# Kernel tuning notes

Measured on AMD Instinct MI355X. Metric: run time of the kernel, lower is better.

## Reference

```python
import jax, jax.numpy as jnp
import numpy as np

N, E, F_IN, F_E, H, T = 100000, 1600000, 128, 16, 64, 32
NEG_SLOPE = 0.2


def setup_inputs() -> dict:
    key = jax.random.key(0)
    ks = jax.random.split(key, 24)
    s = 0.1
    inp = {
        'x': jax.random.normal(ks[0], (N, F_IN), jnp.float32),
        'edge_index': jax.random.randint(ks[1], (2, E), 0, N, dtype=jnp.int32),
        'edge_attr': jax.random.normal(ks[2], (E, F_E), jnp.float32),
        # GATConv layer 1 (heads=1)
        'W1': jax.random.normal(ks[3], (F_IN, H), jnp.float32) * s,
        'as1': jax.random.normal(ks[4], (H,), jnp.float32) * s,
        'ad1': jax.random.normal(ks[5], (H,), jnp.float32) * s,
        'We1': jax.random.normal(ks[6], (F_E, H), jnp.float32) * s,
        'ae1': jax.random.normal(ks[7], (H,), jnp.float32) * s,
        'b1': jnp.zeros((H,), jnp.float32),
        # GATConv layer 2
        'W2': jax.random.normal(ks[8], (H, H), jnp.float32) * s,
        'as2': jax.random.normal(ks[9], (H,), jnp.float32) * s,
        'ad2': jax.random.normal(ks[10], (H,), jnp.float32) * s,
        'We2': jax.random.normal(ks[11], (F_E, H), jnp.float32) * s,
        'ae2': jax.random.normal(ks[12], (H,), jnp.float32) * s,
        'b2': jnp.zeros((H,), jnp.float32),
        # classifier MLP (dropout in eval mode -> identity)
        'Wc1': jax.random.normal(ks[13], (H, H // 2), jnp.float32) * s,
        'bc1': jnp.zeros((H // 2,), jnp.float32),
        'Wc2': jax.random.normal(ks[14], (H // 2, T), jnp.float32) * s,
        'bc2': jnp.zeros((T,), jnp.float32),
    }
    return inp


def gat_conv(x, src, dst, edge_attr, W, a_s, a_d, We, a_e, b):
    """Single-head PyG-style GATConv with edge features and self-loops
    (self-loop edge_attr = mean of incoming edge_attr, fill_value='mean')."""
    n = x.shape[0]
    # self loops with mean incoming edge features
    deg = jax.ops.segment_sum(jnp.ones_like(dst, jnp.float32), dst, n)
    loop_attr = jax.ops.segment_sum(edge_attr, dst, n) / jnp.maximum(deg, 1.0)[:, None]
    loops = jnp.arange(n, dtype=src.dtype)
    src_f = jnp.concatenate([src, loops])
    dst_f = jnp.concatenate([dst, loops])
    ea = jnp.concatenate([edge_attr, loop_attr], axis=0)  # [E+N, F_E]
    h = x @ W                                             # [N, H]
    # attention logits per edge: alpha_src[j] + alpha_dst[i] + alpha_edge
    alpha = (h @ a_s)[src_f] + (h @ a_d)[dst_f] + (ea @ We) @ a_e
    alpha = jax.nn.leaky_relu(alpha, NEG_SLOPE)
    # segment softmax over incoming edges per destination node
    m = jax.ops.segment_max(alpha, dst_f, n)
    p = jnp.exp(alpha - m[dst_f])
    z = jax.ops.segment_sum(p, dst_f, n)
    w = p / z[dst_f]                                      # [E+N]
    out = jax.ops.segment_sum(w[:, None] * h[src_f], dst_f, n)
    return out + b


def reference(x, edge_index, edge_attr, W1, as1, ad1, We1, ae1, b1,
              W2, as2, ad2, We2, ae2, b2, Wc1, bc1, Wc2, bc2):
    src, dst = edge_index[0], edge_index[1]
    h = jax.nn.relu(gat_conv(x, src, dst, edge_attr, W1, as1, ad1, We1, ae1, b1))
    h = jax.nn.relu(gat_conv(h, src, dst, edge_attr, W2, as2, ad2, We2, ae2, b2))
    h = jax.nn.relu(h @ Wc1 + bc1)
    logits = h @ Wc2 + bc2
    return logits
```

## Files before the change

### kernel.cpp

```cpp
#include <hip/hip_runtime.h>
#include <hip/hip_bf16.h>
#include <hip/hip_fp16.h>

#define NEG_SLOPE 0.2f
#define EPB 2048
#define NBUK 512

__device__ __forceinline__ float leaky(float a) { return a > 0.f ? a : NEG_SLOPE * a; }

__global__ __launch_bounds__(256) void count_pack(
    const int* __restrict__ dst, const float* __restrict__ eattr,
    const float* __restrict__ We1, const float* __restrict__ ae1,
    const float* __restrict__ We2, const float* __restrict__ ae2,
    unsigned int* __restrict__ meta_pay, int* __restrict__ counts, int E) {
    __shared__ float wvs[32];
    __shared__ int hist[NBUK];
    int tid = threadIdx.x, i = blockIdx.x;
    if (tid < 32) {
        const float* Wp = (tid < 16) ? We1 : We2;
        const float* ap = (tid < 16) ? ae1 : ae2;
        int f = tid & 15;
        float s = 0.f;
        for (int k = 0; k < 64; ++k) s += Wp[f * 64 + k] * ap[k];
        wvs[tid] = s;
    }
    for (int t = tid; t < NBUK; t += 256) hist[t] = 0;
    __syncthreads();
    int e0 = i * EPB, e1 = min(E, e0 + EPB);
    for (int e = e0 + tid; e < e1; e += 256) {
        int d = dst[e];
        atomicAdd(&hist[d >> 8], 1);
        const float4* ep = (const float4*)(eattr + (size_t)e * 16);
        float4 q0 = ep[0], q1 = ep[1], q2 = ep[2], q3 = ep[3];
        float a[16] = {q0.x, q0.y, q0.z, q0.w, q1.x, q1.y, q1.z, q1.w,
                       q2.x, q2.y, q2.z, q2.w, q3.x, q3.y, q3.z, q3.w};
        float s1 = 0.f, s2 = 0.f;
#pragma unroll
        for (int f = 0; f < 16; ++f) { s1 += a[f] * wvs[f]; s2 += a[f] * wvs[16 + f]; }
        unsigned int p1 = (unsigned int)__half_as_ushort(__float2half_rn(s1));
        unsigned int p2 = (unsigned int)__half_as_ushort(__float2half_rn(s2));
        meta_pay[e] = p1 | (p2 << 16);
    }
    __syncthreads();
    for (int t = tid; t < NBUK; t += 256) counts[(size_t)i * NBUK + t] = hist[t];
}

__global__ __launch_bounds__(1024) void scan_cols(const int* __restrict__ counts,
                                                  int* __restrict__ offsets,
                                                  int* __restrict__ btot, int nblk) {
    __shared__ int sh[1024];
    int b = blockIdx.x, t = threadIdx.x;
    int v = (t < nblk) ? counts[(size_t)t * NBUK + b] : 0;
    sh[t] = v;
    __syncthreads();
    for (int off = 1; off < 1024; off <<= 1) {
        int u = (t >= off) ? sh[t - off] : 0;
        __syncthreads();
        sh[t] += u;
        __syncthreads();
    }
    if (t < nblk) offsets[(size_t)t * NBUK + b] = sh[t] - v;
    if (t == 1023) btot[b] = sh[1023];
}

__global__ void scan_buckets(const int* __restrict__ btot, int* __restrict__ bbase,
                             int* __restrict__ rowptr, int E, int n) {
    __shared__ int sh[NBUK];
    int t = threadIdx.x;
    int v = btot[t];
    sh[t] = v;
    __syncthreads();
    for (int off = 1; off < NBUK; off <<= 1) {
        int u = (t >= off) ? sh[t - off] : 0;
        __syncthreads();
        sh[t] += u;
        __syncthreads();
    }
    bbase[t] = sh[t] - v;
    if (t == 0) rowptr[n] = E;
}

__global__ __launch_bounds__(256) void scatter_buckets(
    const int* __restrict__ dst, const int* __restrict__ src,
    const unsigned int* __restrict__ meta_pay, const int* __restrict__ offsets,
    const int* __restrict__ bbase, uint2* __restrict__ bucketed, int E) {
    __shared__ int cur[NBUK];
    int i = blockIdx.x, tid = threadIdx.x;
    for (int t = tid; t < NBUK; t += 256) cur[t] = bbase[t] + offsets[(size_t)i * NBUK + t];
    __syncthreads();
    int e0 = i * EPB, e1 = min(E, e0 + EPB);
    for (int e = e0 + tid; e < e1; e += 256) {
        int d = dst[e];
        int slot = atomicAdd(&cur[d >> 8], 1);
        bucketed[slot] = make_uint2((unsigned int)src[e] | ((unsigned int)(d & 255) << 24),
                                    meta_pay[e]);
    }
}

__global__ __launch_bounds__(256) void csr_build(const uint2* __restrict__ bucketed,
                                                 const int* __restrict__ bbase,
                                                 const int* __restrict__ btot,
                                                 int* __restrict__ rowptr,
                                                 uint2* __restrict__ recs, int n) {
    __shared__ int deg[256], sc[256], cur[256];
    int b = blockIdx.x, tid = threadIdx.x;
    int base = bbase[b], cnt = btot[b];
    deg[tid] = 0;
    __syncthreads();
    for (int k = tid; k < cnt; k += 256) {
        uint2 r = bucketed[base + k];
        atomicAdd(&deg[r.x >> 24], 1);
    }
    __syncthreads();
    int dv = deg[tid];
    sc[tid] = dv;
    __syncthreads();
    for (int off = 1; off < 256; off <<= 1) {
        int u = (tid >= off) ? sc[tid - off] : 0;
        __syncthreads();
        sc[tid] += u;
        __syncthreads();
    }
    int excl = sc[tid] - dv;
    int d = b * 256 + tid;
    if (d < n) rowptr[d] = base + excl;
    cur[tid] = base + excl;
    __syncthreads();
    for (int k = tid; k < cnt; k += 256) {
        uint2 r = bucketed[base + k];
        int dl = (int)(r.x >> 24);
        int pos = atomicAdd(&cur[dl], 1);
        recs[pos] = make_uint2(r.x & 0x00FFFFFFu, r.y);
    }
}

template <int K>
__global__ __launch_bounds__(256) void gemm_node(const float* __restrict__ X,
                                                 const float* __restrict__ W,
                                                 const float* __restrict__ a_s,
                                                 const float* __restrict__ a_d,
                                                 __half* __restrict__ Hout16,
                                                 float* __restrict__ ash,
                                                 float* __restrict__ adh, int n) {
    constexpr int KC = 64;
    __shared__ float xs[128 * 65];
    __shared__ float ws[KC * 64];
    int tid = threadIdx.x;
    int base = blockIdx.x * 128;
    int ct = tid & 7;
    int rt = tid >> 3;

    float acc[4][8];
#pragma unroll
    for (int i = 0; i < 4; ++i)
#pragma unroll
        for (int j = 0; j < 8; ++j) acc[i][j] = 0.f;

    for (int kc = 0; kc < K; kc += KC) {
#pragma unroll
        for (int p = 0; p < 8; ++p) {
            int idx = p * 256 + tid;
            int row = idx >> 4;
            int f4 = idx & 15;
            float4 q = make_float4(0.f, 0.f, 0.f, 0.f);
            if (base + row < n) q = *(const float4*)(X + (size_t)(base + row) * K + kc + f4 * 4);
            float* dp = xs + row * 65 + f4 * 4;
            dp[0] = q.x; dp[1] = q.y; dp[2] = q.z; dp[3] = q.w;
        }
#pragma unroll
        for (int p = 0; p < 4; ++p) {
            int idx = p * 256 + tid;
            int f = idx >> 4;
            int c4 = idx & 15;
            *(float4*)(ws + f * 64 + c4 * 4) =
                *(const float4*)(W + (size_t)(kc + f) * 64 + c4 * 4);
        }
        __syncthreads();
#pragma unroll 4
        for (int f = 0; f < KC; ++f) {
            float4 w0 = *(const float4*)(ws + f * 64 + ct * 8);
            float4 w1 = *(const float4*)(ws + f * 64 + ct * 8 + 4);
            float b0[8] = {w0.x, w0.y, w0.z, w0.w, w1.x, w1.y, w1.z, w1.w};
#pragma unroll
            for (int i = 0; i < 4; ++i) {
                float a = xs[(rt * 4 + i) * 65 + f];
#pragma unroll
                for (int j = 0; j < 8; ++j) acc[i][j] = fmaf(a, b0[j], acc[i][j]);
            }
        }
        __syncthreads();
    }

    float as_r[8], ad_r[8];
#pragma unroll
    for (int j = 0; j < 8; ++j) { as_r[j] = a_s[ct * 8 + j]; ad_r[j] = a_d[ct * 8 + j]; }
#pragma unroll
    for (int i = 0; i < 4; ++i) {
        int r = base + rt * 4 + i;
        float ps = 0.f, pd = 0.f;
#pragma unroll
        for (int j = 0; j < 8; ++j) {
            ps = fmaf(acc[i][j], as_r[j], ps);
            pd = fmaf(acc[i][j], ad_r[j], pd);
        }
        ps += __shfl_xor(ps, 1); pd += __shfl_xor(pd, 1);
        ps += __shfl_xor(ps, 2); pd += __shfl_xor(pd, 2);
        ps += __shfl_xor(ps, 4); pd += __shfl_xor(pd, 4);
        if (r < n) {
            union { __half h[8]; uint4 u; } pk;
#pragma unroll
            for (int j = 0; j < 8; ++j) pk.h[j] = __float2half_rn(acc[i][j]);
            *(uint4*)(Hout16 + (size_t)r * 64 + ct * 8) = pk.u;
            if (ct == 0) { ash[r] = ps; adh[r] = pd; }
        }
    }
}

template <int LAYER>
__global__ __launch_bounds__(256) void gat_aggregate(
    const __half* __restrict__ Hf, const float* __restrict__ ash, const float* __restrict__ adh,
    const int* __restrict__ rowptr, const uint2* __restrict__ recs,
    const float* __restrict__ bias, float* __restrict__ outp, int n) {
    __shared__ uint2 ops[4][4 * 17];
    int wave = threadIdx.x >> 6;
    int lane = threadIdx.x & 63;
    int gr = lane >> 4;
    int fl = lane & 15;
    int i = blockIdx.x * 16 + wave * 4 + gr;
    if (i >= n) return;
    int start = rowptr[i], end = rowptr[i + 1];
    float adi = adh[i];
    const char* Hb = (const char*)Hf;
    unsigned int fb = (unsigned int)(fl * 8);

    float acc0 = 0.f, acc1 = 0.f, acc2 = 0.f, acc3 = 0.f;
    float zl = 0.f, seal = 0.f;

    for (int c = start; c < end; c += 16) {
        int cnt = min(16, end - c);
        unsigned int o_l = 0;
        float p_l = 0.f;
        if (fl < cnt) {
            uint2 r = recs[c + fl];
            int s_l = (int)r.x;
            o_l = (unsigned int)s_l << 7;
            unsigned short u = (LAYER == 0) ? (unsigned short)(r.y & 0xffffu)
                                            : (unsigned short)(r.y >> 16);
            float e = __half2float(__ushort_as_half(u));
            float p = __expf(leaky(ash[s_l] + adi + e));
            p_l = p;
            zl += p;
            seal += e;
        }
        ops[wave][gr * 17 + fl] = make_uint2(o_l, __float_as_uint(p_l));
        for (int k = 0; k < cnt; ++k) {
            uint2 op = ops[wave][gr * 17 + k];
            uint2 hv = *(const uint2*)(Hb + (op.x + fb));
            float p = __uint_as_float(op.y);
            __half2 h01 = *(__half2*)&hv.x;
            __half2 h23 = *(__half2*)&hv.y;
            acc0 = fmaf(p, __half2float(h01.x), acc0);
            acc1 = fmaf(p, __half2float(h01.y), acc1);
            acc2 = fmaf(p, __half2float(h23.x), acc2);
            acc3 = fmaf(p, __half2float(h23.y), acc3);
        }
    }

#pragma unroll
    for (int off = 1; off < 16; off <<= 1) {
        zl += __shfl_xor(zl, off);
        seal += __shfl_xor(seal, off);
    }

    int d = end - start;
    float loop_sc = seal / (float)max(d, 1);
    float aself = leaky(ash[i] + adi + loop_sc);
    float pself = __expf(aself);
    float z = zl + pself;

    uint2 hvs = *(const uint2*)(Hb + (((unsigned int)i << 7) + fb));
    __half2 s01 = *(__half2*)&hvs.x;
    __half2 s23 = *(__half2*)&hvs.y;
    acc0 = fmaf(pself, __half2float(s01.x), acc0);
    acc1 = fmaf(pself, __half2float(s01.y), acc1);
    acc2 = fmaf(pself, __half2float(s23.x), acc2);
    acc3 = fmaf(pself, __half2float(s23.y), acc3);

    float4 bv = *(const float4*)(bias + fl * 4);
    float4 o;
    o.x = fmaxf(acc0 / z + bv.x, 0.f);
    o.y = fmaxf(acc1 / z + bv.y, 0.f);
    o.z = fmaxf(acc2 / z + bv.z, 0.f);
    o.w = fmaxf(acc3 / z + bv.w, 0.f);
    *(float4*)(outp + (size_t)i * 64 + fl * 4) = o;
}

__global__ __launch_bounds__(256) void mlp_kernel(const float* __restrict__ X,
                                                  const float* __restrict__ Wc1,
                                                  const float* __restrict__ bc1,
                                                  const float* __restrict__ Wc2,
                                                  const float* __restrict__ bc2,
                                                  float* __restrict__ outp, int n) {
    __shared__ float v[8 * 64];
    __shared__ float tb[8 * 32];
    int base = blockIdx.x * 8;
    for (int t = threadIdx.x; t < 512; t += 256) {
        int r = t >> 6;
        v[t] = (base + r < n) ? X[(size_t)base * 64 + t] : 0.f;
    }
    __syncthreads();
    int r = threadIdx.x >> 5, j = threadIdx.x & 31;
    float acc = bc1[j];
#pragma unroll
    for (int k = 0; k < 64; ++k) acc += v[r * 64 + k] * Wc1[k * 32 + j];
    acc = fmaxf(acc, 0.f);
    tb[r * 32 + j] = acc;
    __syncthreads();
    float lg = bc2[j];
#pragma unroll
    for (int k2 = 0; k2 < 32; ++k2) lg += tb[r * 32 + k2] * Wc2[k2 * 32 + j];
    int row = base + r;
    if (row < n) outp[(size_t)row * 32 + j] = lg;
}

extern "C" void kernel_launch(void* const* d_in, const int* in_sizes, int n_in,
                              void* d_out, int out_size, void* d_ws, size_t ws_size,
                              hipStream_t stream) {
    const float* x    = (const float*)d_in[0];
    const int*   ei   = (const int*)d_in[1];
    const float* eatt = (const float*)d_in[2];
    const float* W1   = (const float*)d_in[3];
    const float* as1  = (const float*)d_in[4];
    const float* ad1  = (const float*)d_in[5];
    const float* We1  = (const float*)d_in[6];
    const float* ae1  = (const float*)d_in[7];
    const float* b1   = (const float*)d_in[8];
    const float* W2   = (const float*)d_in[9];
    const float* as2  = (const float*)d_in[10];
    const float* ad2  = (const float*)d_in[11];
    const float* We2  = (const float*)d_in[12];
    const float* ae2  = (const float*)d_in[13];
    const float* b2   = (const float*)d_in[14];
    const float* Wc1  = (const float*)d_in[15];
    const float* bc1  = (const float*)d_in[16];
    const float* Wc2  = (const float*)d_in[17];
    const float* bc2  = (const float*)d_in[18];

    int n = in_sizes[0] / 128;
    int E = in_sizes[1] / 2;
    const int* src = ei;
    const int* dst = ei + E;
    int nblk = (E + EPB - 1) / EPB;

    char* w = (char*)d_ws;
    auto alloc = [&](size_t bytes) { void* p = (void*)w; w += (bytes + 255) & ~(size_t)255; return p; };
    int* rowptr   = (int*)alloc((size_t)(n + 1) * 4);
    int* counts   = (int*)alloc((size_t)nblk * NBUK * 4);
    int* offsets  = (int*)alloc((size_t)nblk * NBUK * 4);
    int* btot     = (int*)alloc((size_t)NBUK * 4);
    int* bbase    = (int*)alloc((size_t)NBUK * 4);
    unsigned int* meta_pay = (unsigned int*)alloc((size_t)E * 4);
    uint2* recs   = (uint2*)alloc((size_t)E * 8);
    __half* hbuf16 = (__half*)alloc((size_t)n * 64 * 2);
    float* obuf   = (float*)alloc((size_t)n * 64 * 4);
    float* ash    = (float*)alloc((size_t)n * 4);
    float* adh    = (float*)alloc((size_t)n * 4);
    uint2* bucketed = (uint2*)obuf;

    count_pack<<<nblk, 256, 0, stream>>>(dst, eatt, We1, ae1, We2, ae2, meta_pay, counts, E);
    scan_cols<<<NBUK, 1024, 0, stream>>>(counts, offsets, btot, nblk);
    scan_buckets<<<1, NBUK, 0, stream>>>(btot, bbase, rowptr, E, n);
    scatter_buckets<<<nblk, 256, 0, stream>>>(dst, src, meta_pay, offsets, bbase, bucketed, E);
    csr_build<<<NBUK, 256, 0, stream>>>(bucketed, bbase, btot, rowptr, recs, n);

    gemm_node<128><<<(n + 127) / 128, 256, 0, stream>>>(x, W1, as1, ad1, hbuf16, ash, adh, n);
    gat_aggregate<0><<<(n + 15) / 16, 256, 0, stream>>>(hbuf16, ash, adh, rowptr, recs, b1, obuf, n);
    gemm_node<64><<<(n + 127) / 128, 256, 0, stream>>>(obuf, W2, as2, ad2, hbuf16, ash, adh, n);
    gat_aggregate<1><<<(n + 15) / 16, 256, 0, stream>>>(hbuf16, ash, adh, rowptr, recs, b2, obuf, n);
    mlp_kernel<<<(n + 7) / 8, 256, 0, stream>>>(obuf, Wc1, bc1, Wc2, bc2, (float*)d_out, n);
}
```

Before: 464.4 us.

## Use MFMA fp16 for node GEMMs and fuse classifier MLP into layer-2 aggregation

Replaces the FP32 shared-memory tiled node GEMM with an MFMA 16x16x32 f16 kernel. Inputs are converted to half on the fly, and a small kernel prepares transposed half weights. The classifier MLP is fused into the second aggregation kernel, with its weights staged in shared memory, which removes one kernel launch and an N×64 float round trip to global memory. The costs are fp16 rounding of the inputs and weights, and a per-block weight load into LDS that raises LDS use in aggregation.

```diff
diff --git a/kernel.cpp b/kernel.cpp
--- a/kernel.cpp
+++ b/kernel.cpp
@@ -6,7 +6,25 @@
 #define EPB 2048
 #define NBUK 512
 
+typedef _Float16 f16x8 __attribute__((ext_vector_type(8)));
+typedef float f32x4 __attribute__((ext_vector_type(4)));
+
 __device__ __forceinline__ float leaky(float a) { return a > 0.f ? a : NEG_SLOPE * a; }
+
+__global__ __launch_bounds__(256) void prep_w(const float* __restrict__ W1,
+                                              const float* __restrict__ W2,
+                                              __half* __restrict__ Wt1,
+                                              __half* __restrict__ Wt2) {
+    int t = threadIdx.x + blockIdx.x * 256;
+    if (t < 8192) {
+        int k = t >> 6, c = t & 63;
+        Wt1[c * 128 + k] = __float2half_rn(W1[t]);
+    } else if (t < 12288) {
+        int i = t - 8192;
+        int k = i >> 6, c = i & 63;
+        Wt2[c * 64 + k] = __float2half_rn(W2[i]);
+    }
+}
 
 __global__ __launch_bounds__(256) void count_pack(
     const int* __restrict__ dst, const float* __restrict__ eattr,
@@ -135,84 +153,59 @@
 }
 
 template <int K>
-__global__ __launch_bounds__(256) void gemm_node(const float* __restrict__ X,
-                                                 const float* __restrict__ W,
-                                                 const float* __restrict__ a_s,
-                                                 const float* __restrict__ a_d,
-                                                 __half* __restrict__ Hout16,
-                                                 float* __restrict__ ash,
-                                                 float* __restrict__ adh, int n) {
-    constexpr int KC = 64;
-    __shared__ float xs[128 * 65];
-    __shared__ float ws[KC * 64];
+__global__ __launch_bounds__(256) void gemm_node_mfma(
+    const float* __restrict__ X, const __half* __restrict__ Wt,
+    const float* __restrict__ a_s, const float* __restrict__ a_d,
+    __half* __restrict__ Hout16, float* __restrict__ ash, float* __restrict__ adh, int n) {
     int tid = threadIdx.x;
-    int base = blockIdx.x * 128;
-    int ct = tid & 7;
-    int rt = tid >> 3;
-
-    float acc[4][8];
-#pragma unroll
-    for (int i = 0; i < 4; ++i)
-#pragma unroll
-        for (int j = 0; j < 8; ++j) acc[i][j] = 0.f;
-
-    for (int kc = 0; kc < K; kc += KC) {
-#pragma unroll
-        for (int p = 0; p < 8; ++p) {
-            int idx = p * 256 + tid;
-            int row = idx >> 4;
-            int f4 = idx & 15;
-            float4 q = make_float4(0.f, 0.f, 0.f, 0.f);
-            if (base + row < n) q = *(const float4*)(X + (size_t)(base + row) * K + kc + f4 * 4);
-            float* dp = xs + row * 65 + f4 * 4;
-            dp[0] = q.x; dp[1] = q.y; dp[2] = q.z; dp[3] = q.w;
-        }
-#pragma unroll
-        for (int p = 0; p < 4; ++p) {
-            int idx = p * 256 + tid;
-            int f = idx >> 4;
-            int c4 = idx & 15;
-            *(float4*)(ws + f * 64 + c4 * 4) =
-                *(const float4*)(W + (size_t)(kc + f) * 64 + c4 * 4);
-        }
-        __syncthreads();
-#pragma unroll 4
-        for (int f = 0; f < KC; ++f) {
-            float4 w0 = *(const float4*)(ws + f * 64 + ct * 8);
-            float4 w1 = *(const float4*)(ws + f * 64 + ct * 8 + 4);
-            float b0[8] = {w0.x, w0.y, w0.z, w0.w, w1.x, w1.y, w1.z, w1.w};
-#pragma unroll
-            for (int i = 0; i < 4; ++i) {
-                float a = xs[(rt * 4 + i) * 65 + f];
-#pragma unroll
-                for (int j = 0; j < 8; ++j) acc[i][j] = fmaf(a, b0[j], acc[i][j]);
-            }
-        }
-        __syncthreads();
-    }
-
-    float as_r[8], ad_r[8];
-#pragma unroll
-    for (int j = 0; j < 8; ++j) { as_r[j] = a_s[ct * 8 + j]; ad_r[j] = a_d[ct * 8 + j]; }
-#pragma unroll
-    for (int i = 0; i < 4; ++i) {
-        int r = base + rt * 4 + i;
-        float ps = 0.f, pd = 0.f;
-#pragma unroll
-        for (int j = 0; j < 8; ++j) {
-            ps = fmaf(acc[i][j], as_r[j], ps);
-            pd = fmaf(acc[i][j], ad_r[j], pd);
-        }
-        ps += __shfl_xor(ps, 1); pd += __shfl_xor(pd, 1);
-        ps += __shfl_xor(ps, 2); pd += __shfl_xor(pd, 2);
-        ps += __shfl_xor(ps, 4); pd += __shfl_xor(pd, 4);
-        if (r < n) {
-            union { __half h[8]; uint4 u; } pk;
-#pragma unroll
-            for (int j = 0; j < 8; ++j) pk.h[j] = __float2half_rn(acc[i][j]);
-            *(uint4*)(Hout16 + (size_t)r * 64 + ct * 8) = pk.u;
-            if (ct == 0) { ash[r] = ps; adh[r] = pd; }
-        }
+    int wave = tid >> 6, lane = tid & 63;
+    int g = lane >> 4, q15 = lane & 15;
+    int node = blockIdx.x * 64 + wave * 16 + q15;
+    int nodec = min(node, n - 1);
+    const float* xrow = X + (size_t)nodec * K + g * 8;
+    const _Float16* wbase = (const _Float16*)Wt + (size_t)q15 * K + g * 8;
+
+    f32x4 acc[4];
+#pragma unroll
+    for (int t = 0; t < 4; ++t) acc[t] = (f32x4){0.f, 0.f, 0.f, 0.f};
+
+#pragma unroll
+    for (int kk = 0; kk < K / 32; ++kk) {
+        float4 xa = *(const float4*)(xrow + kk * 32);
+        float4 xc = *(const float4*)(xrow + kk * 32 + 4);
+        f16x8 xb;
+        xb[0] = (_Float16)xa.x; xb[1] = (_Float16)xa.y;
+        xb[2] = (_Float16)xa.z; xb[3] = (_Float16)xa.w;
+        xb[4] = (_Float16)xc.x; xb[5] = (_Float16)xc.y;
+        xb[6] = (_Float16)xc.z; xb[7] = (_Float16)xc.w;
+#pragma unroll
+        for (int t = 0; t < 4; ++t) {
+            f16x8 wa = *(const f16x8*)(wbase + t * 16 * K + kk * 32);
+            acc[t] = __builtin_amdgcn_mfma_f32_16x16x32_f16(wa, xb, acc[t], 0, 0, 0);
+        }
+    }
+
+    float ps = 0.f, pd = 0.f;
+#pragma unroll
+    for (int t = 0; t < 4; ++t)
+#pragma unroll
+        for (int r = 0; r < 4; ++r) {
+            int f = t * 16 + g * 4 + r;
+            ps = fmaf(acc[t][r], a_s[f], ps);
+            pd = fmaf(acc[t][r], a_d[f], pd);
+        }
+    ps += __shfl_xor(ps, 16); pd += __shfl_xor(pd, 16);
+    ps += __shfl_xor(ps, 32); pd += __shfl_xor(pd, 32);
+
+    if (node < n) {
+#pragma unroll
+        for (int t = 0; t < 4; ++t) {
+            union { _Float16 h[4]; uint2 u2; } pk;
+#pragma unroll
+            for (int r = 0; r < 4; ++r) pk.h[r] = (_Float16)acc[t][r];
+            *(uint2*)(Hout16 + (size_t)node * 64 + t * 16 + g * 4) = pk.u2;
+        }
+        if (g == 0) { ash[node] = ps; adh[node] = pd; }
     }
 }
 
@@ -220,16 +213,31 @@
 __global__ __launch_bounds__(256) void gat_aggregate(
     const __half* __restrict__ Hf, const float* __restrict__ ash, const float* __restrict__ adh,
     const int* __restrict__ rowptr, const uint2* __restrict__ recs,
-    const float* __restrict__ bias, float* __restrict__ outp, int n) {
+    const float* __restrict__ bias,
+    const float* __restrict__ Wc1, const float* __restrict__ bc1,
+    const float* __restrict__ Wc2, const float* __restrict__ bc2,
+    float* __restrict__ outp, int n) {
     __shared__ uint2 ops[4][4 * 17];
+    __shared__ float mlpbuf[LAYER ? (2048 + 1024 + 64 + 1024 + 512) : 1];
+
+    if (LAYER == 1) {
+        for (int t = threadIdx.x; t < 2048; t += 256) mlpbuf[t] = Wc1[t];
+        for (int t = threadIdx.x; t < 1024; t += 256) mlpbuf[2048 + t] = Wc2[t];
+        if (threadIdx.x < 32) mlpbuf[3072 + threadIdx.x] = bc1[threadIdx.x];
+        else if (threadIdx.x < 64) mlpbuf[3072 + threadIdx.x] = bc2[threadIdx.x - 32];
+        __syncthreads();
+    }
+
     int wave = threadIdx.x >> 6;
     int lane = threadIdx.x & 63;
     int gr = lane >> 4;
     int fl = lane & 15;
     int i = blockIdx.x * 16 + wave * 4 + gr;
-    if (i >= n) return;
-    int start = rowptr[i], end = rowptr[i + 1];
-    float adi = adh[i];
+    bool valid = i < n;
+    int ic = valid ? i : 0;
+    int start = 0, end = 0;
+    if (valid) { start = rowptr[i]; end = rowptr[i + 1]; }
+    float adi = adh[ic];
     const char* Hb = (const char*)Hf;
     unsigned int fb = (unsigned int)(fl * 8);
 
@@ -266,61 +274,63 @@
         }
     }
 
-#pragma unroll
-    for (int off = 1; off < 16; off <<= 1) {
-        zl += __shfl_xor(zl, off);
-        seal += __shfl_xor(seal, off);
-    }
-
-    int d = end - start;
-    float loop_sc = seal / (float)max(d, 1);
-    float aself = leaky(ash[i] + adi + loop_sc);
-    float pself = __expf(aself);
-    float z = zl + pself;
-
-    uint2 hvs = *(const uint2*)(Hb + (((unsigned int)i << 7) + fb));
-    __half2 s01 = *(__half2*)&hvs.x;
-    __half2 s23 = *(__half2*)&hvs.y;
-    acc0 = fmaf(pself, __half2float(s01.x), acc0);
-    acc1 = fmaf(pself, __half2float(s01.y), acc1);
-    acc2 = fmaf(pself, __half2float(s23.x), acc2);
-    acc3 = fmaf(pself, __half2float(s23.y), acc3);
-
-    float4 bv = *(const float4*)(bias + fl * 4);
-    float4 o;
-    o.x = fmaxf(acc0 / z + bv.x, 0.f);
-    o.y = fmaxf(acc1 / z + bv.y, 0.f);
-    o.z = fmaxf(acc2 / z + bv.z, 0.f);
-    o.w = fmaxf(acc3 / z + bv.w, 0.f);
-    *(float4*)(outp + (size_t)i * 64 + fl * 4) = o;
-}
-
-__global__ __launch_bounds__(256) void mlp_kernel(const float* __restrict__ X,
-                                                  const float* __restrict__ Wc1,
-                                                  const float* __restrict__ bc1,
-                                                  const float* __restrict__ Wc2,
-                                                  const float* __restrict__ bc2,
-                                                  float* __restrict__ outp, int n) {
-    __shared__ float v[8 * 64];
-    __shared__ float tb[8 * 32];
-    int base = blockIdx.x * 8;
-    for (int t = threadIdx.x; t < 512; t += 256) {
-        int r = t >> 6;
-        v[t] = (base + r < n) ? X[(size_t)base * 64 + t] : 0.f;
-    }
-    __syncthreads();
-    int r = threadIdx.x >> 5, j = threadIdx.x & 31;
-    float acc = bc1[j];
-#pragma unroll
-    for (int k = 0; k < 64; ++k) acc += v[r * 64 + k] * Wc1[k * 32 + j];
-    acc = fmaxf(acc, 0.f);
-    tb[r * 32 + j] = acc;
-    __syncthreads();
-    float lg = bc2[j];
-#pragma unroll
-    for (int k2 = 0; k2 < 32; ++k2) lg += tb[r * 32 + k2] * Wc2[k2 * 32 + j];
-    int row = base + r;
-    if (row < n) outp[(size_t)row * 32 + j] = lg;
+    if (valid) {
+#pragma unroll
+        for (int off = 1; off < 16; off <<= 1) {
+            zl += __shfl_xor(zl, off);
+            seal += __shfl_xor(seal, off);
+        }
+        int d = end - start;
+        float loop_sc = seal / (float)max(d, 1);
+        float aself = leaky(ash[ic] + adi + loop_sc);
+        float pself = __expf(aself);
+        float z = zl + pself;
+
+        uint2 hvs = *(const uint2*)(Hb + (((unsigned int)ic << 7) + fb));
+        __half2 s01 = *(__half2*)&hvs.x;
+        __half2 s23 = *(__half2*)&hvs.y;
+        acc0 = fmaf(pself, __half2float(s01.x), acc0);
+        acc1 = fmaf(pself, __half2float(s01.y), acc1);
+        acc2 = fmaf(pself, __half2float(s23.x), acc2);
+        acc3 = fmaf(pself, __half2float(s23.y), acc3);
+
+        float4 bv = *(const float4*)(bias + fl * 4);
+        float4 o;
+        o.x = fmaxf(acc0 / z + bv.x, 0.f);
+        o.y = fmaxf(acc1 / z + bv.y, 0.f);
+        o.z = fmaxf(acc2 / z + bv.z, 0.f);
+        o.w = fmaxf(acc3 / z + bv.w, 0.f);
+
+        if (LAYER == 0) {
+            *(float4*)(outp + (size_t)i * 64 + fl * 4) = o;
+        } else {
+            float* wc1s = mlpbuf;
+            float* wc2s = mlpbuf + 2048;
+            float* bcs = mlpbuf + 3072;
+            float* o_row = mlpbuf + 3136 + (wave * 4 + gr) * 64;
+            float* t1row = mlpbuf + 3136 + 1024 + (wave * 4 + gr) * 32;
+            *(float4*)(o_row + fl * 4) = o;
+            float s0 = bcs[fl * 2], s1 = bcs[fl * 2 + 1];
+#pragma unroll 8
+            for (int k = 0; k < 64; ++k) {
+                float ov = o_row[k];
+                s0 = fmaf(ov, wc1s[k * 32 + fl * 2], s0);
+                s1 = fmaf(ov, wc1s[k * 32 + fl * 2 + 1], s1);
+            }
+            s0 = fmaxf(s0, 0.f);
+            s1 = fmaxf(s1, 0.f);
+            t1row[fl * 2] = s0;
+            t1row[fl * 2 + 1] = s1;
+            float l0 = bcs[32 + fl * 2], l1 = bcs[32 + fl * 2 + 1];
+#pragma unroll 8
+            for (int k = 0; k < 32; ++k) {
+                float tv = t1row[k];
+                l0 = fmaf(tv, wc2s[k * 32 + fl * 2], l0);
+                l1 = fmaf(tv, wc2s[k * 32 + fl * 2 + 1], l1);
+            }
+            *(float2*)(outp + (size_t)i * 32 + fl * 2) = make_float2(l0, l1);
+        }
+    }
 }
 
 extern "C" void kernel_launch(void* const* d_in, const int* in_sizes, int n_in,
@@ -365,7 +375,11 @@
     float* obuf   = (float*)alloc((size_t)n * 64 * 4);
     float* ash    = (float*)alloc((size_t)n * 4);
     float* adh    = (float*)alloc((size_t)n * 4);
+    __half* Wt1   = (__half*)alloc(64 * 128 * 2);
+    __half* Wt2   = (__half*)alloc(64 * 64 * 2);
     uint2* bucketed = (uint2*)obuf;
+
+    prep_w<<<48, 256, 0, stream>>>(W1, W2, Wt1, Wt2);
 
     count_pack<<<nblk, 256, 0, stream>>>(dst, eatt, We1, ae1, We2, ae2, meta_pay, counts, E);
     scan_cols<<<NBUK, 1024, 0, stream>>>(counts, offsets, btot, nblk);
@@ -373,9 +387,10 @@
     scatter_buckets<<<nblk, 256, 0, stream>>>(dst, src, meta_pay, offsets, bbase, bucketed, E);
     csr_build<<<NBUK, 256, 0, stream>>>(bucketed, bbase, btot, rowptr, recs, n);
 
-    gemm_node<128><<<(n + 127) / 128, 256, 0, stream>>>(x, W1, as1, ad1, hbuf16, ash, adh, n);
-    gat_aggregate<0><<<(n + 15) / 16, 256, 0, stream>>>(hbuf16, ash, adh, rowptr, recs, b1, obuf, n);
-    gemm_node<64><<<(n + 127) / 128, 256, 0, stream>>>(obuf, W2, as2, ad2, hbuf16, ash, adh, n);
-    gat_aggregate<1><<<(n + 15) / 16, 256, 0, stream>>>(hbuf16, ash, adh, rowptr, recs, b2, obuf, n);
-    mlp_kernel<<<(n + 7) / 8, 256, 0, stream>>>(obuf, Wc1, bc1, Wc2, bc2, (float*)d_out, n);
-}
+    gemm_node_mfma<128><<<(n + 63) / 64, 256, 0, stream>>>(x, Wt1, as1, ad1, hbuf16, ash, adh, n);
+    gat_aggregate<0><<<(n + 15) / 16, 256, 0, stream>>>(hbuf16, ash, adh, rowptr, recs, b1,
+                                                        nullptr, nullptr, nullptr, nullptr, obuf, n);
+    gemm_node_mfma<64><<<(n + 63) / 64, 256, 0, stream>>>(obuf, Wt2, as2, ad2, hbuf16, ash, adh, n);
+    gat_aggregate<1><<<(n + 15) / 16, 256, 0, stream>>>(hbuf16, ash, adh, rowptr, recs, b2,
+                                                        Wc1, bc1, Wc2, bc2, (float*)d_out, n);
+}
```

Result: faster. 433.7 us (-6.6%).
